# Kernel optimization log

Measured on AMD Instinct MI355X. Metric: run time of the kernel, lower is better.

The kernel has to match this reference:

```python
import jax, jax.numpy as jnp
import numpy as np

V = 50000   # vocab_size
D = 128     # embed_dim
B = 2048    # number of (center, contexts) pairs
C = 20      # context window size


def setup_inputs() -> dict:
    key = jax.random.key(0)
    ks = jax.random.split(key, 12)
    s = 0.05
    inp = {
        "center_id": jax.random.randint(ks[0], (B,), 0, V),
        "context_ids": jax.random.randint(ks[1], (B, C), 0, V),
        "epsilon": jax.random.normal(ks[2], (D,), dtype=jnp.float32),
        # parameters (torch Linear convention: W is [out, in])
        "embeddings": jax.random.normal(ks[3], (V, D), dtype=jnp.float32) * s,
        "prior_locs": jax.random.normal(ks[4], (V, D), dtype=jnp.float32) * s,
        "prior_scales": jax.random.normal(ks[5], (V, D), dtype=jnp.float32) * s,
        "W_enc": jax.random.normal(ks[6], (2 * D, 2 * D), dtype=jnp.float32) * s,
        "b_enc": jnp.zeros((2 * D,), dtype=jnp.float32),
        "W_loc": jax.random.normal(ks[7], (D, 2 * D), dtype=jnp.float32) * s,
        "b_loc": jnp.zeros((D,), dtype=jnp.float32),
        "W_scale": jax.random.normal(ks[8], (D, 2 * D), dtype=jnp.float32) * s,
        "b_scale": jnp.zeros((D,), dtype=jnp.float32),
        "W_vocab": jax.random.normal(ks[9], (V, D), dtype=jnp.float32) * s,
        "b_vocab": jnp.zeros((V,), dtype=jnp.float32),
    }
    return inp


def reference(center_id, context_ids, epsilon, embeddings, prior_locs, prior_scales,
              W_enc, b_enc, W_loc, b_loc, W_scale, b_scale, W_vocab, b_vocab):
    # Embedding lookups
    center_embed = embeddings[center_id]              # [B, D]
    context_embeds = embeddings[context_ids]          # [B, C, D]
    center_rep = jnp.broadcast_to(center_embed[:, None, :], context_embeds.shape)
    enc_in = jnp.concatenate([center_rep, context_embeds], axis=2)  # [B, C, 2D]

    # Encoder + sum over context
    h = jax.nn.relu(jnp.einsum('bcd,ed->bce', enc_in, W_enc) + b_enc)
    h = jnp.sum(h, axis=1)                            # [B, 2D]

    loc = h @ W_loc.T + b_loc                         # [B, D]
    scale = jax.nn.softplus(h @ W_scale.T + b_scale)  # [B, D]

    # Reparameterized sample (single shared epsilon, as in original)
    z = loc + scale * epsilon                         # [B, D]

    # Categorical over vocab; log-softmax == log(softmax) stably
    logits = z @ W_vocab.T + b_vocab                  # [B, V]
    log_cat = jax.nn.log_softmax(logits, axis=1)

    # Log-likelihood: sum_k log p(context_k | z)  (vectorized gather-reduce)
    lls = jnp.take_along_axis(log_cat, context_ids, axis=1).sum(axis=1)  # [B]

    # Closed-form diagonal-Gaussian KL( N(loc, scale^2) || N(ploc, pscale^2) )
    prior_loc = prior_locs[center_id]
    prior_scale = jax.nn.softplus(prior_scales[center_id])
    var0 = scale ** 2
    var1 = prior_scale ** 2
    kl = jnp.sum(jnp.log(prior_scale / scale) + (var0 + (loc - prior_loc) ** 2) / (2.0 * var1) - 0.5,
                 axis=1)                              # [B]

    elbo = lls - kl
    return jnp.mean(-elbo)
```

## Files before the change

kernel.cpp:

```cpp
#include <hip/hip_runtime.h>
#include <math.h>

#define VSZ 50000
#define VPAD 50048
#define DD  128
#define BB  2048
#define CC  20
#define E2  256

#define NCHK 98
#define CH_COLS 512
#define NRB 16
#define NWG (NCHK * NRB)

typedef short short8 __attribute__((ext_vector_type(8)));
typedef float f32x4  __attribute__((ext_vector_type(4)));

#define LOG2E 1.44269504f

__device__ __forceinline__ float softplusf(float x) {
  if (x > 20.f) return x;
  if (x < -20.f) return __expf(x);
  return log1pf(__expf(x));
}

__device__ __forceinline__ unsigned short f2bf(float f) {
  unsigned u = __float_as_uint(f);
  u = (u + 0x7fffu + ((u >> 16) & 1u)) >> 16;
  return (unsigned short)u;
}

__device__ __forceinline__ short8 pack8(float4 x, float4 y) {
  short8 r;
  r[0] = (short)f2bf(x.x); r[1] = (short)f2bf(x.y);
  r[2] = (short)f2bf(x.z); r[3] = (short)f2bf(x.w);
  r[4] = (short)f2bf(y.x); r[5] = (short)f2bf(y.y);
  r[6] = (short)f2bf(y.z); r[7] = (short)f2bf(y.w);
  return r;
}

__device__ __forceinline__ void gload_lds16(const void* g, void* l) {
  __builtin_amdgcn_global_load_lds(
      (const __attribute__((address_space(1))) unsigned int*)g,
      (__attribute__((address_space(3))) unsigned int*)l, 16, 0, 0);
}

#define NV4 1600000
#define NE4 16384
#define NL4 8192
__global__ __launch_bounds__(256) void convert_all_kernel(
    const float* __restrict__ Wv, const float* __restrict__ We,
    const float* __restrict__ Wl, const float* __restrict__ Wsc,
    ushort4* __restrict__ wv_bf, ushort4* __restrict__ we_bf,
    ushort4* __restrict__ wls_bf, float* __restrict__ S)
{
  const int gtid = blockIdx.x * 256 + threadIdx.x;
  if (gtid < BB) S[gtid] = 0.f;
  if (gtid < (VPAD - VSZ) * 32) {
    ushort4 z; z.x = 0; z.y = 0; z.z = 0; z.w = 0;
    wv_bf[(size_t)VSZ * 32 + gtid] = z;
  }
  const int total = NV4 + NE4 + 2 * NL4;
  const int stride = gridDim.x * 256;
  for (int idx = gtid; idx < total; idx += stride) {
    const float4* src; ushort4* dst; int off;
    if (idx < NV4)                   { src = (const float4*)Wv;  dst = wv_bf;  off = idx; }
    else if (idx < NV4 + NE4)        { src = (const float4*)We;  dst = we_bf;  off = idx - NV4; }
    else if (idx < NV4 + NE4 + NL4)  { src = (const float4*)Wl;  dst = wls_bf; off = idx - NV4 - NE4; }
    else { src = (const float4*)Wsc; dst = wls_bf + NL4;         off = idx - NV4 - NE4 - NL4; }
    float4 v = src[off];
    ushort4 o;
    o.x = f2bf(v.x); o.y = f2bf(v.y); o.z = f2bf(v.z); o.w = f2bf(v.w);
    dst[off] = o;
  }
}

__global__ __launch_bounds__(256) void enc_mfma_kernel(
    const int* __restrict__ center_id, const int* __restrict__ context_ids,
    const float* __restrict__ embeddings,
    const unsigned short* __restrict__ we_bf, const float* __restrict__ b_enc,
    unsigned short* __restrict__ h_bf)
{
  const int b    = blockIdx.x;
  const int tid  = threadIdx.x;
  const int wave = tid >> 6, lane = tid & 63;
  const int lr = lane & 15;
  const int lk = lane >> 4;

  const int cid   = center_id[b];
  const int row1  = 16 + lr;
  const int ctx0  = context_ids[b * CC + lr];
  const int ctx1  = (row1 < CC) ? context_ids[b * CC + row1] : 0;
  const bool r1ok = (row1 < CC);

  f32x4 acc[2][4];
  #pragma unroll
  for (int rt = 0; rt < 2; rt++)
    #pragma unroll
    for (int ct = 0; ct < 4; ct++) acc[rt][ct] = (f32x4){0.f, 0.f, 0.f, 0.f};

  #pragma unroll
  for (int step = 0; step < 4; step++) {
    const int k0 = step * 32 + lk * 8;
    const float4* p = (const float4*)(embeddings + (size_t)cid * DD + k0);
    short8 a = pack8(p[0], p[1]);
    #pragma unroll
    for (int ct = 0; ct < 4; ct++) {
      const int e = (wave * 4 + ct) * 16 + lr;
      short8 w = *(const short8*)(we_bf + (size_t)e * E2 + k0);
      acc[0][ct] = __builtin_amdgcn_mfma_f32_16x16x32_bf16(a, w, acc[0][ct], 0, 0, 0);
      acc[1][ct] = __builtin_amdgcn_mfma_f32_16x16x32_bf16(a, w, acc[1][ct], 0, 0, 0);
    }
  }
  #pragma unroll
  for (int step = 4; step < 8; step++) {
    const int k0 = step * 32 + lk * 8;
    const int kk = k0 - DD;
    const float4* p0 = (const float4*)(embeddings + (size_t)ctx0 * DD + kk);
    short8 a0 = pack8(p0[0], p0[1]);
    short8 a1 = (short8)0;
    if (r1ok) {
      const float4* p1 = (const float4*)(embeddings + (size_t)ctx1 * DD + kk);
      a1 = pack8(p1[0], p1[1]);
    }
    #pragma unroll
    for (int ct = 0; ct < 4; ct++) {
      const int e = (wave * 4 + ct) * 16 + lr;
      short8 w = *(const short8*)(we_bf + (size_t)e * E2 + k0);
      acc[0][ct] = __builtin_amdgcn_mfma_f32_16x16x32_bf16(a0, w, acc[0][ct], 0, 0, 0);
      acc[1][ct] = __builtin_amdgcn_mfma_f32_16x16x32_bf16(a1, w, acc[1][ct], 0, 0, 0);
    }
  }

  float be[4], p[4];
  #pragma unroll
  for (int ct = 0; ct < 4; ct++) { be[ct] = b_enc[(wave * 4 + ct) * 16 + lr]; p[ct] = 0.f; }
  #pragma unroll
  for (int rt = 0; rt < 2; rt++) {
    #pragma unroll
    for (int j = 0; j < 4; j++) {
      const int row = rt * 16 + lk * 4 + j;
      if (row < CC) {
        #pragma unroll
        for (int ct = 0; ct < 4; ct++) p[ct] += fmaxf(acc[rt][ct][j] + be[ct], 0.f);
      }
    }
  }
  #pragma unroll
  for (int ct = 0; ct < 4; ct++) {
    p[ct] += __shfl_xor(p[ct], 16);
    p[ct] += __shfl_xor(p[ct], 32);
  }
  if (lk == 0) {
    #pragma unroll
    for (int ct = 0; ct < 4; ct++)
      h_bf[(size_t)b * E2 + (wave * 4 + ct) * 16 + lr] = f2bf(p[ct]);
  }
}

__global__ __launch_bounds__(256) void ls_post_kernel(
    const int* __restrict__ center_id, const int* __restrict__ context_ids,
    const float* __restrict__ eps,
    const float* __restrict__ prior_locs, const float* __restrict__ prior_scales,
    const unsigned short* __restrict__ h_bf, const unsigned short* __restrict__ wls_bf,
    const float* __restrict__ b_loc, const float* __restrict__ b_scale,
    const float* __restrict__ W_vocab, const float* __restrict__ b_vocab,
    unsigned short* __restrict__ zbf, float* __restrict__ base)
{
  const int b0   = blockIdx.x * 8;
  const int tid  = threadIdx.x;
  const int wave = tid >> 6, lane = tid & 63;
  const int lr = lane & 15, lk = lane >> 4;

  __shared__ __align__(16) float loc_s[8][DD];
  __shared__ __align__(16) float scale_s[8][DD];
  __shared__ __align__(16) float zsh[8][DD];
  __shared__ float klv[8], ctxacc[8];

  if (tid < 8) ctxacc[tid] = 0.f;

  f32x4 acc[4];
  #pragma unroll
  for (int ct = 0; ct < 4; ct++) acc[ct] = (f32x4){0.f, 0.f, 0.f, 0.f};

  #pragma unroll
  for (int step = 0; step < 8; step++) {
    const int k0 = step * 32 + lk * 8;
    short8 a = (lr < 8) ? *(const short8*)(h_bf + (size_t)(b0 + lr) * E2 + k0) : (short8)0;
    #pragma unroll
    for (int ct = 0; ct < 4; ct++) {
      const int o = (wave * 4 + ct) * 16 + lr;
      short8 w = *(const short8*)(wls_bf + (size_t)o * E2 + k0);
      acc[ct] = __builtin_amdgcn_mfma_f32_16x16x32_bf16(a, w, acc[ct], 0, 0, 0);
    }
  }
  #pragma unroll
  for (int ct = 0; ct < 4; ct++) {
    const int o = (wave * 4 + ct) * 16 + lr;
    #pragma unroll
    for (int j = 0; j < 4; j++) {
      const int br = lk * 4 + j;
      if (br < 8) {
        const float v = acc[ct][j];
        if (o < DD) loc_s[br][o] = v + b_loc[o];
        else        scale_s[br][o - DD] = softplusf(v + b_scale[o - DD]);
      }
    }
  }
  __syncthreads();

  if (tid < 128) {
    const int bi = tid >> 4, d0 = (tid & 15) * 8;
    const int cid = center_id[b0 + bi];
    const float* pl = prior_locs  + (size_t)cid * DD + d0;
    const float* ps = prior_scales + (size_t)cid * DD + d0;
    float kacc = 0.f;
    short8 zb;
    #pragma unroll
    for (int q = 0; q < 8; q++) {
      const float loc = loc_s[bi][d0 + q], scl = scale_s[bi][d0 + q];
      const float z = fmaf(scl, eps[d0 + q], loc);
      zsh[bi][d0 + q] = z;
      zb[q] = (short)f2bf(z);
      const float ploc = pl[q];
      const float pscl = softplusf(ps[q]);
      const float dd = loc - ploc;
      kacc += logf(pscl / scl) + (scl * scl + dd * dd) / (2.f * pscl * pscl) - 0.5f;
    }
    *(short8*)(zbf + (size_t)(b0 + bi) * DD + d0) = zb;
    #pragma unroll
    for (int off = 1; off < 16; off <<= 1) kacc += __shfl_xor(kacc, off, 16);
    if ((tid & 15) == 0) klv[bi] = kacc;
  }
  __syncthreads();

  for (int idx = tid; idx < 8 * CC; idx += 256) {
    const int db = idx / CC, c = idx - db * CC;
    const int vid = context_ids[(size_t)(b0 + db) * CC + c];
    const float4* wv = (const float4*)(W_vocab + (size_t)vid * DD);
    const float4* zz = (const float4*)(&zsh[db][0]);
    float dsum = b_vocab[vid];
    #pragma unroll 8
    for (int q = 0; q < DD / 4; q++) {
      float4 w = wv[q], z4 = zz[q];
      dsum = fmaf(w.x, z4.x, dsum); dsum = fmaf(w.y, z4.y, dsum);
      dsum = fmaf(w.z, z4.z, dsum); dsum = fmaf(w.w, z4.w, dsum);
    }
    atomicAdd(&ctxacc[db], dsum);
  }
  __syncthreads();

  if (tid < 8) base[b0 + tid] = klv[tid] - ctxacc[tid];
}

__global__ __launch_bounds__(256, 4) void logits_mfma_kernel(
    const unsigned short* __restrict__ zbf, const unsigned short* __restrict__ wbf,
    const float* __restrict__ b_vocab, float* __restrict__ S)
{
  __shared__ __align__(16) char lds[2][16384];

  const int tid  = threadIdx.x;
  const int wave = tid >> 6, lane = tid & 63;
  const int lr = lane & 15;
  const int lk = lane >> 4;

  const int swz = (blockIdx.x & 7) * (NWG / 8) + (blockIdx.x >> 3);
  const int ch  = swz >> 4;
  const int rb  = swz & 15;
  const int nst = (ch == NCHK - 1) ? 6 : 8;
  const size_t cbase = (size_t)ch * CH_COLS * 256;
  const int row0 = rb * 128 + wave * 32;

  short8 a[2][4];
  #pragma unroll
  for (int rt = 0; rt < 2; rt++)
    #pragma unroll
    for (int kk = 0; kk < 4; kk++)
      a[rt][kk] = *(const short8*)(zbf + (size_t)(row0 + rt * 16 + lr) * DD + kk * 32 + lk * 8);

#define STAGE(buf, st) do {                                                    \
    _Pragma("unroll")                                                          \
    for (int i_ = 0; i_ < 4; i_++) {                                           \
      const int c_ = (wave * 4 + i_) * 4 + (lane >> 4);                        \
      const size_t go_ = cbase + (size_t)(st) * 16384 +                        \
                         (size_t)c_ * 256 + (size_t)(((lane & 15) ^ (c_ & 15)) << 4); \
      gload_lds16((const char*)wbf + go_, &lds[(buf)][(wave * 4 + i_) * 1024]);\
    }                                                                          \
  } while (0)

  STAGE(0, 0);

  float Ssum[2][4];
  #pragma unroll
  for (int rt = 0; rt < 2; rt++)
    #pragma unroll
    for (int j = 0; j < 4; j++) Ssum[rt][j] = 0.f;

  __syncthreads();

  for (int step = 0; step < nst; step++) {
    const int buf = step & 1;
    if (step + 1 < nst) STAGE(buf ^ 1, step + 1);

    float ebv[4];
    #pragma unroll
    for (int ct = 0; ct < 4; ct++) {
      const int g = ch * CH_COLS + step * 64 + ct * 16 + lr;
      const float bv = b_vocab[g < VSZ ? g : (VSZ - 1)];
      ebv[ct] = (g < VSZ) ? exp2f(bv * LOG2E) : 0.f;
    }

    const char* lb = &lds[buf][0];
    f32x4 acc[2][4];
    #pragma unroll
    for (int ct = 0; ct < 4; ct++) {
      acc[0][ct] = (f32x4){0.f, 0.f, 0.f, 0.f};
      acc[1][ct] = (f32x4){0.f, 0.f, 0.f, 0.f};
      short8 bf[4];
      #pragma unroll
      for (int kk = 0; kk < 4; kk++)
        bf[kk] = *(const short8*)(lb + (ct * 16 + lr) * 256 + (((kk * 4 + lk) ^ lr) << 4));
      #pragma unroll
      for (int kk = 0; kk < 4; kk++) {
        acc[0][ct] = __builtin_amdgcn_mfma_f32_16x16x32_bf16(a[0][kk], bf[kk], acc[0][ct], 0, 0, 0);
        acc[1][ct] = __builtin_amdgcn_mfma_f32_16x16x32_bf16(a[1][kk], bf[kk], acc[1][ct], 0, 0, 0);
      }
    }

    #pragma unroll
    for (int rt = 0; rt < 2; rt++)
      #pragma unroll
      for (int ct = 0; ct < 4; ct++)
        #pragma unroll
        for (int j = 0; j < 4; j++)
          Ssum[rt][j] = fmaf(exp2f(acc[rt][ct][j] * LOG2E), ebv[ct], Ssum[rt][j]);

    __syncthreads();
  }
#undef STAGE

  #pragma unroll
  for (int rt = 0; rt < 2; rt++)
    #pragma unroll
    for (int j = 0; j < 4; j++) {
      float s = Ssum[rt][j];
      s += __shfl_xor(s, 1, 16);
      s += __shfl_xor(s, 2, 16);
      s += __shfl_xor(s, 4, 16);
      s += __shfl_xor(s, 8, 16);
      if (lr == 0) atomicAdd(&S[row0 + rt * 16 + lk * 4 + j], s);
    }
}

__global__ __launch_bounds__(256) void fin_kernel(
    const float* __restrict__ S, const float* __restrict__ base, float* __restrict__ out)
{
  const int t = threadIdx.x;
  float local = 0.f;
  for (int b = t; b < BB; b += 256)
    local += base[b] + (float)CC * logf(S[b]);
  __shared__ float red[256];
  red[t] = local;
  __syncthreads();
  for (int off = 128; off; off >>= 1) {
    if (t < off) red[t] += red[t + off];
    __syncthreads();
  }
  if (t == 0) out[0] = red[0] / (float)BB;
}

extern "C" void kernel_launch(void* const* d_in, const int* in_sizes, int n_in,
                              void* d_out, int out_size, void* d_ws, size_t ws_size,
                              hipStream_t stream) {
  const int*   center_id    = (const int*)d_in[0];
  const int*   context_ids  = (const int*)d_in[1];
  const float* eps          = (const float*)d_in[2];
  const float* embeddings   = (const float*)d_in[3];
  const float* prior_locs   = (const float*)d_in[4];
  const float* prior_scales = (const float*)d_in[5];
  const float* W_enc        = (const float*)d_in[6];
  const float* b_enc        = (const float*)d_in[7];
  const float* W_loc        = (const float*)d_in[8];
  const float* b_loc        = (const float*)d_in[9];
  const float* W_scale      = (const float*)d_in[10];
  const float* b_scale      = (const float*)d_in[11];
  const float* W_vocab      = (const float*)d_in[12];
  const float* b_vocab      = (const float*)d_in[13];
  float* out = (float*)d_out;

  char* ws = (char*)d_ws;
  unsigned short* wv_bf  = (unsigned short*)(ws);
  unsigned short* we_bf  = (unsigned short*)(ws + 12812288);
  unsigned short* wls_bf = (unsigned short*)(ws + 12812288 + 131072);
  unsigned short* h_bf   = (unsigned short*)(ws + 12812288 + 2 * 131072);
  unsigned short* zbf    = (unsigned short*)(ws + 12812288 + 2 * 131072 + 1048576);
  float*          S      = (float*)(ws + 12812288 + 2 * 131072 + 1048576 + 524288);
  float*          base   = (float*)(ws + 12812288 + 2 * 131072 + 1048576 + 524288 + 8192);

  hipLaunchKernelGGL(convert_all_kernel, dim3(512), dim3(256), 0, stream,
                     W_vocab, W_enc, W_loc, W_scale,
                     (ushort4*)wv_bf, (ushort4*)we_bf, (ushort4*)wls_bf, S);
  hipLaunchKernelGGL(enc_mfma_kernel, dim3(BB), dim3(256), 0, stream,
                     center_id, context_ids, embeddings, we_bf, b_enc, h_bf);
  hipLaunchKernelGGL(ls_post_kernel, dim3(BB / 8), dim3(256), 0, stream,
                     center_id, context_ids, eps, prior_locs, prior_scales,
                     h_bf, wls_bf, b_loc, b_scale, W_vocab, b_vocab, zbf, base);
  hipLaunchKernelGGL(logits_mfma_kernel, dim3(NWG), dim3(256), 0, stream,
                     zbf, wv_bf, b_vocab, S);
  hipLaunchKernelGGL(fin_kernel, dim3(1), dim3(256), 0, stream, S, base, out);
}
```

Before: 133.6 us.

## Enlarge logits tile rows, triple-buffer LDS, precompute exp(bias) table and fold log2e

The logits kernel now covers 256 rows per workgroup instead of 128, which halves the number of workgroups and the reloads of W_vocab tiles. LDS staging moves from double to triple buffering, with explicit vmcnt waits and raw barriers in a fully unrolled loop. exp(b_vocab) is precomputed once as a bf16 table in the convert kernel, and log2e is folded into the bf16 z values so the inner loop needs no multiply. In exchange, the padded vocab grows to a whole number of chunks, occupancy drops to 3 waves per SIMD, register pressure rises, and storing exp(bias) in bf16 loses some precision.

```diff
diff --git a/kernel.cpp b/kernel.cpp
--- a/kernel.cpp
+++ b/kernel.cpp
@@ -2,7 +2,7 @@
 #include <math.h>
 
 #define VSZ 50000
-#define VPAD 50048
+#define VPAD 50176
 #define DD  128
 #define BB  2048
 #define CC  20
@@ -10,7 +10,7 @@
 
 #define NCHK 98
 #define CH_COLS 512
-#define NRB 16
+#define NRB 8
 #define NWG (NCHK * NRB)
 
 typedef short short8 __attribute__((ext_vector_type(8)));
@@ -51,17 +51,27 @@
 __global__ __launch_bounds__(256) void convert_all_kernel(
     const float* __restrict__ Wv, const float* __restrict__ We,
     const float* __restrict__ Wl, const float* __restrict__ Wsc,
+    const float* __restrict__ b_vocab,
     ushort4* __restrict__ wv_bf, ushort4* __restrict__ we_bf,
-    ushort4* __restrict__ wls_bf, float* __restrict__ S)
+    ushort4* __restrict__ wls_bf, unsigned short* __restrict__ ebv_tab,
+    float* __restrict__ S)
 {
   const int gtid = blockIdx.x * 256 + threadIdx.x;
+  const int stride = gridDim.x * 256;
   if (gtid < BB) S[gtid] = 0.f;
   if (gtid < (VPAD - VSZ) * 32) {
     ushort4 z; z.x = 0; z.y = 0; z.z = 0; z.w = 0;
     wv_bf[(size_t)VSZ * 32 + gtid] = z;
   }
+  for (int idx = gtid; idx < NCHK * 512; idx += stride) {
+    const int ch = idx >> 9, r = idx & 511;
+    const int lr = r >> 5, q = r & 31, st = q >> 2, ct = q & 3;
+    const int g = ch * CH_COLS + st * 64 + ct * 16 + lr;
+    float ev = 0.f;
+    if (g < VSZ) ev = exp2f(b_vocab[g] * LOG2E);
+    ebv_tab[idx] = f2bf(ev);
+  }
   const int total = NV4 + NE4 + 2 * NL4;
-  const int stride = gridDim.x * 256;
   for (int idx = gtid; idx < total; idx += stride) {
     const float4* src; ushort4* dst; int off;
     if (idx < NV4)                   { src = (const float4*)Wv;  dst = wv_bf;  off = idx; }
@@ -221,7 +231,7 @@
       const float loc = loc_s[bi][d0 + q], scl = scale_s[bi][d0 + q];
       const float z = fmaf(scl, eps[d0 + q], loc);
       zsh[bi][d0 + q] = z;
-      zb[q] = (short)f2bf(z);
+      zb[q] = (short)f2bf(z * LOG2E);
       const float ploc = pl[q];
       const float pscl = softplusf(ps[q]);
       const float dd = loc - ploc;
@@ -253,11 +263,11 @@
   if (tid < 8) base[b0 + tid] = klv[tid] - ctxacc[tid];
 }
 
-__global__ __launch_bounds__(256, 4) void logits_mfma_kernel(
+__global__ __launch_bounds__(256, 3) void logits_mfma_kernel(
     const unsigned short* __restrict__ zbf, const unsigned short* __restrict__ wbf,
-    const float* __restrict__ b_vocab, float* __restrict__ S)
+    const unsigned short* __restrict__ ebv_tab, float* __restrict__ S)
 {
-  __shared__ __align__(16) char lds[2][16384];
+  __shared__ __align__(16) char lds[3][16384];
 
   const int tid  = threadIdx.x;
   const int wave = tid >> 6, lane = tid & 63;
@@ -265,15 +275,23 @@
   const int lk = lane >> 4;
 
   const int swz = (blockIdx.x & 7) * (NWG / 8) + (blockIdx.x >> 3);
-  const int ch  = swz >> 4;
-  const int rb  = swz & 15;
-  const int nst = (ch == NCHK - 1) ? 6 : 8;
-  const size_t cbase = (size_t)ch * CH_COLS * 256;
-  const int row0 = rb * 128 + wave * 32;
-
-  short8 a[2][4];
-  #pragma unroll
-  for (int rt = 0; rt < 2; rt++)
+  const int ch  = swz >> 3;
+  const int rb  = swz & 7;
+  const size_t cbase = (size_t)ch * (CH_COLS * 256);
+  const int row0 = rb * 256 + wave * 64;
+
+  unsigned int ew[16];
+  {
+    const uint4* tp = (const uint4*)(ebv_tab + ((size_t)ch * 16 + lr) * 32);
+    *(uint4*)(ew + 0)  = tp[0];
+    *(uint4*)(ew + 4)  = tp[1];
+    *(uint4*)(ew + 8)  = tp[2];
+    *(uint4*)(ew + 12) = tp[3];
+  }
+
+  short8 a[4][4];
+  #pragma unroll
+  for (int rt = 0; rt < 4; rt++)
     #pragma unroll
     for (int kk = 0; kk < 4; kk++)
       a[rt][kk] = *(const short8*)(zbf + (size_t)(row0 + rt * 16 + lr) * DD + kk * 32 + lk * 8);
@@ -289,58 +307,57 @@
   } while (0)
 
   STAGE(0, 0);
-
-  float Ssum[2][4];
-  #pragma unroll
-  for (int rt = 0; rt < 2; rt++)
+  STAGE(1, 1);
+
+  float Ssum[4][4];
+  #pragma unroll
+  for (int rt = 0; rt < 4; rt++)
     #pragma unroll
     for (int j = 0; j < 4; j++) Ssum[rt][j] = 0.f;
 
-  __syncthreads();
-
-  for (int step = 0; step < nst; step++) {
-    const int buf = step & 1;
-    if (step + 1 < nst) STAGE(buf ^ 1, step + 1);
-
-    float ebv[4];
+  #pragma unroll
+  for (int t = 0; t < 8; t++) {
+    if (t < 7) asm volatile("s_waitcnt vmcnt(4)" ::: "memory");
+    else       asm volatile("s_waitcnt vmcnt(0)" ::: "memory");
+    __builtin_amdgcn_s_barrier();
+    __builtin_amdgcn_sched_barrier(0);
+    if (t + 2 < 8) STAGE((t + 2) % 3, t + 2);
+
+    float ev[4];
+    {
+      const unsigned w0 = ew[2 * t], w1 = ew[2 * t + 1];
+      ev[0] = __uint_as_float(w0 << 16);
+      ev[1] = __uint_as_float(w0 & 0xffff0000u);
+      ev[2] = __uint_as_float(w1 << 16);
+      ev[3] = __uint_as_float(w1 & 0xffff0000u);
+    }
+
+    const char* lb = &lds[t % 3][0];
     #pragma unroll
     for (int ct = 0; ct < 4; ct++) {
-      const int g = ch * CH_COLS + step * 64 + ct * 16 + lr;
-      const float bv = b_vocab[g < VSZ ? g : (VSZ - 1)];
-      ebv[ct] = (g < VSZ) ? exp2f(bv * LOG2E) : 0.f;
-    }
-
-    const char* lb = &lds[buf][0];
-    f32x4 acc[2][4];
-    #pragma unroll
-    for (int ct = 0; ct < 4; ct++) {
-      acc[0][ct] = (f32x4){0.f, 0.f, 0.f, 0.f};
-      acc[1][ct] = (f32x4){0.f, 0.f, 0.f, 0.f};
       short8 bf[4];
       #pragma unroll
       for (int kk = 0; kk < 4; kk++)
         bf[kk] = *(const short8*)(lb + (ct * 16 + lr) * 256 + (((kk * 4 + lk) ^ lr) << 4));
+      f32x4 acc[4];
       #pragma unroll
-      for (int kk = 0; kk < 4; kk++) {
-        acc[0][ct] = __builtin_amdgcn_mfma_f32_16x16x32_bf16(a[0][kk], bf[kk], acc[0][ct], 0, 0, 0);
-        acc[1][ct] = __builtin_amdgcn_mfma_f32_16x16x32_bf16(a[1][kk], bf[kk], acc[1][ct], 0, 0, 0);
-      }
-    }
-
-    #pragma unroll
-    for (int rt = 0; rt < 2; rt++)
+      for (int rt = 0; rt < 4; rt++) acc[rt] = (f32x4){0.f, 0.f, 0.f, 0.f};
       #pragma unroll
-      for (int ct = 0; ct < 4; ct++)
+      for (int kk = 0; kk < 4; kk++)
+        #pragma unroll
+        for (int rt = 0; rt < 4; rt++)
+          acc[rt] = __builtin_amdgcn_mfma_f32_16x16x32_bf16(a[rt][kk], bf[kk], acc[rt], 0, 0, 0);
+      #pragma unroll
+      for (int rt = 0; rt < 4; rt++)
         #pragma unroll
         for (int j = 0; j < 4; j++)
-          Ssum[rt][j] = fmaf(exp2f(acc[rt][ct][j] * LOG2E), ebv[ct], Ssum[rt][j]);
-
-    __syncthreads();
+          Ssum[rt][j] = fmaf(exp2f(acc[rt][j]), ev[ct], Ssum[rt][j]);
+    }
   }
 #undef STAGE
 
   #pragma unroll
-  for (int rt = 0; rt < 2; rt++)
+  for (int rt = 0; rt < 4; rt++)
     #pragma unroll
     for (int j = 0; j < 4; j++) {
       float s = Ssum[rt][j];
@@ -390,22 +407,23 @@
 
   char* ws = (char*)d_ws;
   unsigned short* wv_bf  = (unsigned short*)(ws);
-  unsigned short* we_bf  = (unsigned short*)(ws + 12812288);
-  unsigned short* wls_bf = (unsigned short*)(ws + 12812288 + 131072);
-  unsigned short* h_bf   = (unsigned short*)(ws + 12812288 + 2 * 131072);
-  unsigned short* zbf    = (unsigned short*)(ws + 12812288 + 2 * 131072 + 1048576);
-  float*          S      = (float*)(ws + 12812288 + 2 * 131072 + 1048576 + 524288);
-  float*          base   = (float*)(ws + 12812288 + 2 * 131072 + 1048576 + 524288 + 8192);
+  unsigned short* we_bf  = (unsigned short*)(ws + 12845056);
+  unsigned short* wls_bf = (unsigned short*)(ws + 12845056 + 131072);
+  unsigned short* h_bf   = (unsigned short*)(ws + 12845056 + 2 * 131072);
+  unsigned short* zbf    = (unsigned short*)(ws + 12845056 + 2 * 131072 + 1048576);
+  float*          S      = (float*)(ws + 12845056 + 2 * 131072 + 1048576 + 524288);
+  float*          base   = (float*)(ws + 12845056 + 2 * 131072 + 1048576 + 524288 + 8192);
+  unsigned short* ebv    = (unsigned short*)(ws + 12845056 + 2 * 131072 + 1048576 + 524288 + 2 * 8192);
 
   hipLaunchKernelGGL(convert_all_kernel, dim3(512), dim3(256), 0, stream,
-                     W_vocab, W_enc, W_loc, W_scale,
-                     (ushort4*)wv_bf, (ushort4*)we_bf, (ushort4*)wls_bf, S);
+                     W_vocab, W_enc, W_loc, W_scale, b_vocab,
+                     (ushort4*)wv_bf, (ushort4*)we_bf, (ushort4*)wls_bf, ebv, S);
   hipLaunchKernelGGL(enc_mfma_kernel, dim3(BB), dim3(256), 0, stream,
                      center_id, context_ids, embeddings, we_bf, b_enc, h_bf);
   hipLaunchKernelGGL(ls_post_kernel, dim3(BB / 8), dim3(256), 0, stream,
                      center_id, context_ids, eps, prior_locs, prior_scales,
                      h_bf, wls_bf, b_loc, b_scale, W_vocab, b_vocab, zbf, base);
   hipLaunchKernelGGL(logits_mfma_kernel, dim3(NWG), dim3(256), 0, stream,
-                     zbf, wv_bf, b_vocab, S);
+                     zbf, wv_bf, ebv, S);
   hipLaunchKernelGGL(fin_kernel, dim3(1), dim3(256), 0, stream, S, base, out);
 }
```

After: 390.1 us. 2.92x slower.
